# Kernel tuning notes

Measured on AMD Instinct MI355X. Metric: run time of the kernel, lower is better.

## Reference

```python
import jax, jax.numpy as jnp
import numpy as np

N = 100000       # nodes
E = 1600000      # edges (avg degree 16)
IN_DIM = 64
HID_DIM = 128
OUT_DIM = 64

def setup_inputs() -> dict:
    key = jax.random.key(0)
    k = jax.random.split(key, 8)
    inp = jax.random.normal(k[0], (IN_DIM, N), dtype=jnp.float32)
    src = jax.random.randint(k[1], (E,), 0, N, dtype=jnp.int32)
    dst = jax.random.randint(k[2], (E,), 0, N, dtype=jnp.int32)
    # Linear params (torch nn.Linear: y = x @ W.T + b)
    s1 = 1.0 / np.sqrt(IN_DIM)
    W1 = jax.random.uniform(k[3], (HID_DIM, IN_DIM), jnp.float32, -s1, s1)
    b1 = jax.random.uniform(k[4], (HID_DIM,), jnp.float32, -s1, s1)
    s2 = 1.0 / np.sqrt(HID_DIM)
    W2 = jax.random.uniform(k[5], (OUT_DIM, HID_DIM), jnp.float32, -s2, s2)
    b2 = jax.random.uniform(k[6], (OUT_DIM,), jnp.float32, -s2, s2)
    return {"inp": inp, "src": src, "dst": dst, "W1": W1, "b1": b1, "W2": W2, "b2": b2}

def reference(inp, src, dst, W1, b1, W2, b2):
    # inp: [in_dim, N] (module passes transposed features)
    X = inp.T                                   # [N, in_dim] node features
    # update_all(copy_src, sum): gather src features, scatter-add at dst
    agg = jax.ops.segment_sum(X[src], dst, num_segments=X.shape[0])  # [N, in_dim]
    h = jax.nn.relu(agg @ W1.T + b1)            # [N, hidden]
    out = h @ W2.T + b2                         # [N, out_dim]
    return out.T                                 # [out_dim, N] (final .t())
```

## Files before the change

### kernel.cpp

```cpp
#include <hip/hip_runtime.h>
#include <hip/hip_bf16.h>
#include <stdint.h>

typedef unsigned short ushort_t;
using short8   = __attribute__((ext_vector_type(8))) short;
using float4v  = __attribute__((ext_vector_type(4))) float;

#define BSH    6
#define BUCKW  64
#define CAP    1536
#define NBMAX  2048
#define TPITCH 266
#define BINB   128

__device__ __forceinline__ float bf2f(ushort_t u) {
    union { unsigned int i; float f; } v;
    v.i = ((unsigned int)u) << 16;
    return v.f;
}
__device__ __forceinline__ ushort_t f2b(float f) {
    union { float f; unsigned int i; } v;
    v.f = f;
    unsigned int u = v.i;
    unsigned int r = (u + 0x7fffu + ((u >> 16) & 1u)) >> 16;
    return (ushort_t)r;
}
__device__ __forceinline__ float blo2f(unsigned v) {
    union { unsigned i; float f; } u; u.i = v << 16; return u.f;
}
__device__ __forceinline__ float bhi2f(unsigned v) {
    union { unsigned i; float f; } u; u.i = v & 0xFFFF0000u; return u.f;
}

__global__ __launch_bounds__(1024) void prep_k(
        const float* __restrict__ inp, ushort_t* __restrict__ X, int N,
        const float* __restrict__ W1, const float* __restrict__ W2,
        ushort_t* __restrict__ w1b, ushort_t* __restrict__ w2b,
        const int* __restrict__ src, const int* __restrict__ dst,
        int* __restrict__ gcur, unsigned* __restrict__ bin, int E,
        int NB, int TB) {
    __shared__ __align__(16) char smem[64 * TPITCH * 2];
    int tid = threadIdx.x;

    if ((int)blockIdx.x < TB) {
        if (blockIdx.x == 0) {
            for (int i = tid; i < 8192; i += 1024) {
                w1b[i] = f2b(W1[i]);
                w2b[i] = f2b(W2[i]);
            }
        }
        ushort_t* tile = (ushort_t*)smem;
        int w    = tid >> 6;
        int lane = tid & 63;
        int n0   = blockIdx.x * 256;
        int col  = (w >> 2) * 64 + lane;
        int nc   = n0 + col;
#pragma unroll
        for (int r = 0; r < 16; ++r) {
            int d = (w & 3) * 16 + r;
            if (nc < N) tile[d * TPITCH + col] = f2b(inp[(size_t)d * N + nc]);
        }
        __syncthreads();
#pragma unroll
        for (int r = 0; r < 16; ++r) {
            int nl = w * 16 + r;
            int n  = n0 + nl;
            if (n < N) X[(size_t)n * 64 + lane] = tile[lane * TPITCH + nl];
        }
    } else {
        int* lcnt  = (int*)smem;
        int* gbase = lcnt + NBMAX;
        int* lcur  = gbase + NBMAX;
        int bid   = blockIdx.x - TB;
        int chunk = (E + BINB - 1) / BINB;
        int s0 = bid * chunk;
        int s1 = s0 + chunk;
        if (s1 > E) s1 = E;

        for (int b = tid; b < NB; b += 1024) lcnt[b] = 0;
        __syncthreads();

        for (int e = s0 + tid; e < s1; e += 1024)
            atomicAdd(&lcnt[dst[e] >> BSH], 1);
        __syncthreads();

        for (int b = tid; b < NB; b += 1024) {
            int c = lcnt[b];
            gbase[b] = c ? atomicAdd(&gcur[b], c) : 0;
            lcur[b]  = 0;
        }
        __syncthreads();

        for (int e = s0 + tid; e < s1; e += 1024) {
            int d = dst[e];
            int b = d >> BSH;
            int pos = gbase[b] + atomicAdd(&lcur[b], 1);
            if (pos < CAP)
                bin[(size_t)b * CAP + pos] =
                    ((unsigned)(d & (BUCKW - 1)) << 24) | (unsigned)src[e];
        }
    }
}

__global__ __launch_bounds__(256) void bagg_k(
        const unsigned* __restrict__ Xu, const unsigned* __restrict__ bin,
        const int* __restrict__ gcur, unsigned* __restrict__ aggu, int N) {
    __shared__ unsigned sl[CAP];
    __shared__ int ecnt[BUCKW];
    __shared__ int sc[BUCKW];
    __shared__ int ecur[BUCKW];
    int tid = threadIdx.x;
    int b   = blockIdx.x;
    int lo  = b << BSH;

    int cnt = gcur[b];
    if (cnt > CAP) cnt = CAP;
    const unsigned* bb = bin + (size_t)b * CAP;

    if (tid < BUCKW) ecnt[tid] = 0;
    __syncthreads();

    for (int i = tid; i < cnt; i += 256)
        atomicAdd(&ecnt[bb[i] >> 24], 1);
    __syncthreads();

    if (tid < BUCKW) sc[tid] = ecnt[tid];
    __syncthreads();
#pragma unroll
    for (int off = 1; off < BUCKW; off <<= 1) {
        int v = 0;
        if (tid < BUCKW && tid >= off) v = sc[tid - off];
        __syncthreads();
        if (tid < BUCKW) sc[tid] += v;
        __syncthreads();
    }
    if (tid < BUCKW) { sc[tid] -= ecnt[tid]; ecur[tid] = 0; }
    __syncthreads();

    for (int i = tid; i < cnt; i += 256) {
        unsigned p = bb[i];
        int nl  = (int)(p >> 24);
        int pos = sc[nl] + atomicAdd(&ecur[nl], 1);
        sl[pos] = p;
    }
    __syncthreads();

    int wave = tid >> 6;
    int lane = tid & 63;
    int half = lane >> 5;
    int c2   = lane & 31;

    for (int n = wave; n < BUCKW; n += 4) {
        int node = lo + n;
        if (node >= N) break;
        int s0 = sc[n];
        int c  = ecnt[n];
        float alo0 = 0.f, ahi0 = 0.f, alo1 = 0.f, ahi1 = 0.f;
        int i = 0;
        for (; i + 16 <= c; i += 16) {
            unsigned p0 = sl[s0 + i +  0 + half], p1 = sl[s0 + i +  2 + half];
            unsigned p2 = sl[s0 + i +  4 + half], p3 = sl[s0 + i +  6 + half];
            unsigned p4 = sl[s0 + i +  8 + half], p5 = sl[s0 + i + 10 + half];
            unsigned p6 = sl[s0 + i + 12 + half], p7 = sl[s0 + i + 14 + half];
            unsigned v0 = Xu[(size_t)(p0 & 0xFFFFFFu) * 32 + c2];
            unsigned v1 = Xu[(size_t)(p1 & 0xFFFFFFu) * 32 + c2];
            unsigned v2 = Xu[(size_t)(p2 & 0xFFFFFFu) * 32 + c2];
            unsigned v3 = Xu[(size_t)(p3 & 0xFFFFFFu) * 32 + c2];
            unsigned v4 = Xu[(size_t)(p4 & 0xFFFFFFu) * 32 + c2];
            unsigned v5 = Xu[(size_t)(p5 & 0xFFFFFFu) * 32 + c2];
            unsigned v6 = Xu[(size_t)(p6 & 0xFFFFFFu) * 32 + c2];
            unsigned v7 = Xu[(size_t)(p7 & 0xFFFFFFu) * 32 + c2];
            alo0 += blo2f(v0); ahi0 += bhi2f(v0);
            alo1 += blo2f(v1); ahi1 += bhi2f(v1);
            alo0 += blo2f(v2); ahi0 += bhi2f(v2);
            alo1 += blo2f(v3); ahi1 += bhi2f(v3);
            alo0 += blo2f(v4); ahi0 += bhi2f(v4);
            alo1 += blo2f(v5); ahi1 += bhi2f(v5);
            alo0 += blo2f(v6); ahi0 += bhi2f(v6);
            alo1 += blo2f(v7); ahi1 += bhi2f(v7);
        }
        for (; i + 2 <= c; i += 2) {
            unsigned p = sl[s0 + i + half];
            unsigned v = Xu[(size_t)(p & 0xFFFFFFu) * 32 + c2];
            alo0 += blo2f(v); ahi0 += bhi2f(v);
        }
        if (i + half < c) {
            unsigned p = sl[s0 + i + half];
            unsigned v = Xu[(size_t)(p & 0xFFFFFFu) * 32 + c2];
            alo1 += blo2f(v); ahi1 += bhi2f(v);
        }
        float alo = alo0 + alo1;
        float ahi = ahi0 + ahi1;
        float blo = __shfl(alo, lane + 32);
        float bhi = __shfl(ahi, lane + 32);
        if (half == 0) {
            alo += blo; ahi += bhi;
            aggu[(size_t)node * 32 + c2] =
                (unsigned)f2b(alo) | ((unsigned)f2b(ahi) << 16);
        }
    }
}

#define HPITCH 136

__global__ __launch_bounds__(256) void mlp_k(
        const ushort_t* __restrict__ aggb,
        const ushort_t* __restrict__ W1, const float* __restrict__ b1,
        const ushort_t* __restrict__ W2, const float* __restrict__ b2,
        float* __restrict__ out, int N) {
    __shared__ ushort_t h_s[4][16 * HPITCH];

    int wave = threadIdx.x >> 6;
    int lane = threadIdx.x & 63;
    int row  = lane & 15;
    int quad = lane >> 4;
    int n0   = blockIdx.x * 64 + wave * 16;

    int anode = n0 + row;
    if (anode > N - 1) anode = N - 1;
    const ushort_t* ap = aggb + (size_t)anode * 64;
    short8 a0 = *(const short8*)(ap + quad * 8);
    short8 a1 = *(const short8*)(ap + 32 + quad * 8);

    float4v zero = {0.f, 0.f, 0.f, 0.f};
    float4v acc[8];
#pragma unroll
    for (int nt = 0; nt < 8; ++nt) acc[nt] = zero;

#pragma unroll
    for (int nt = 0; nt < 8; ++nt) {
        const ushort_t* wp = W1 + (size_t)(nt * 16 + row) * 64 + quad * 8;
        short8 bf0 = *(const short8*)(wp);
        short8 bf1 = *(const short8*)(wp + 32);
        acc[nt] = __builtin_amdgcn_mfma_f32_16x16x32_bf16(a0, bf0, acc[nt], 0, 0, 0);
        acc[nt] = __builtin_amdgcn_mfma_f32_16x16x32_bf16(a1, bf1, acc[nt], 0, 0, 0);
    }

    ushort_t* hw = h_s[wave];
#pragma unroll
    for (int nt = 0; nt < 8; ++nt) {
        float bias = b1[nt * 16 + row];
#pragma unroll
        for (int r = 0; r < 4; ++r) {
            float v = acc[nt][r] + bias;
            v = v > 0.f ? v : 0.f;
            hw[(quad * 4 + r) * HPITCH + nt * 16 + row] = f2b(v);
        }
    }
    __syncthreads();

    short8 a2[4];
#pragma unroll
    for (int kt = 0; kt < 4; ++kt)
        a2[kt] = *(const short8*)(hw + row * HPITCH + kt * 32 + quad * 8);

    float4v acc2[4];
#pragma unroll
    for (int nt = 0; nt < 4; ++nt) acc2[nt] = zero;

#pragma unroll
    for (int nt = 0; nt < 4; ++nt) {
#pragma unroll
        for (int kt = 0; kt < 4; ++kt) {
            short8 bfr = *(const short8*)(W2 + (size_t)(nt * 16 + row) * 128 +
                                          kt * 32 + quad * 8);
            acc2[nt] = __builtin_amdgcn_mfma_f32_16x16x32_bf16(a2[kt], bfr, acc2[nt], 0, 0, 0);
        }
    }

    int node = n0 + quad * 4;
    if (node < N) {
#pragma unroll
        for (int nt = 0; nt < 4; ++nt) {
            int ko = nt * 16 + row;
            float bias = b2[ko];
            float4v pk;
#pragma unroll
            for (int r = 0; r < 4; ++r) pk[r] = acc2[nt][r] + bias;
            *(float4v*)(out + (size_t)ko * N + node) = pk;
        }
    }
}

extern "C" void kernel_launch(void* const* d_in, const int* in_sizes, int n_in,
                              void* d_out, int out_size, void* d_ws, size_t ws_size,
                              hipStream_t stream) {
    const float* inp = (const float*)d_in[0];
    const int*   src = (const int*)d_in[1];
    const int*   dst = (const int*)d_in[2];
    const float* W1  = (const float*)d_in[3];
    const float* b1  = (const float*)d_in[4];
    const float* W2  = (const float*)d_in[5];
    const float* b2  = (const float*)d_in[6];
    float* out = (float*)d_out;

    int N  = in_sizes[0] / 64;
    int E  = in_sizes[1];
    int NB = (N + BUCKW - 1) >> BSH;

    ushort_t* aggb = (ushort_t*)d_ws;
    ushort_t* w1b  = aggb + (size_t)N * 64;
    ushort_t* w2b  = w1b + 8192;
    int*      gcur = (int*)(w2b + 8192);

    char*     ob  = (char*)d_out;
    ushort_t* X   = (ushort_t*)ob;
    unsigned* bin = (unsigned*)(ob + (size_t)N * 64 * 2);

    hipMemsetAsync(gcur, 0, NB * sizeof(int), stream);

    int TB = (N + 255) / 256;
    prep_k<<<TB + BINB, 1024, 0, stream>>>(inp, X, N, W1, W2, w1b, w2b,
                                           src, dst, gcur, bin, E, NB, TB);

    bagg_k<<<NB, 256, 0, stream>>>((const unsigned*)X, bin, gcur,
                                   (unsigned*)aggb, N);

    int tb = (N + 63) / 64;
    mlp_k<<<tb, 256, 0, stream>>>(aggb, w1b, b1, w2b, b2, out, N);
}
```

Measured before the change: 204.1 us.

## Fuse aggregation with MLP via shared-memory tile and split prep kernels

Merges the bucket aggregation kernel with the MLP kernel, so each 64-node bucket's aggregated features go to LDS and feed the MFMA layers straight away instead of round-tripping through global memory. The transpose and binning work are split into separate kernels, and the memset is replaced by initialising gcur to absolute per-bucket offsets. This removes one global write and read of the aggregated features and one launch. In exchange, the binning no longer overlaps with the transpose, and the fused kernel's LDS use and register pressure grow.

```diff
diff --git a/kernel.cpp b/kernel.cpp
--- a/kernel.cpp
+++ b/kernel.cpp
@@ -10,8 +10,8 @@
 #define BUCKW  64
 #define CAP    1536
 #define NBMAX  2048
-#define TPITCH 266
-#define BINB   128
+#define HPITCH 136
+#define APITCH 72
 
 __device__ __forceinline__ float bf2f(ushort_t u) {
     union { unsigned int i; float f; } v;
@@ -32,92 +32,99 @@
     union { unsigned i; float f; } u; u.i = v & 0xFFFF0000u; return u.f;
 }
 
-__global__ __launch_bounds__(1024) void prep_k(
-        const float* __restrict__ inp, ushort_t* __restrict__ X, int N,
-        const float* __restrict__ W1, const float* __restrict__ W2,
-        ushort_t* __restrict__ w1b, ushort_t* __restrict__ w2b,
+__global__ void transpose_k(const float* __restrict__ inp,
+                            ushort_t* __restrict__ X, int N,
+                            const float* __restrict__ W1,
+                            const float* __restrict__ W2,
+                            ushort_t* __restrict__ w1b,
+                            ushort_t* __restrict__ w2b,
+                            int* __restrict__ gcur, int NB) {
+    if (blockIdx.x == 0) {
+        for (int i = threadIdx.x; i < 8192; i += 256) {
+            w1b[i] = f2b(W1[i]);
+            w2b[i] = f2b(W2[i]);
+        }
+        for (int b = threadIdx.x; b < NB; b += 256) gcur[b] = b * CAP;
+    }
+    __shared__ float tile[64][65];
+    int tx = threadIdx.x & 63;
+    int ty = threadIdx.x >> 6;
+    int n0 = blockIdx.x * 64;
+#pragma unroll
+    for (int r = 0; r < 16; ++r) {
+        int d = ty * 16 + r;
+        int n = n0 + tx;
+        if (n < N) tile[d][tx] = inp[(size_t)d * N + n];
+    }
+    __syncthreads();
+#pragma unroll
+    for (int r = 0; r < 16; ++r) {
+        int nl = ty * 16 + r;
+        int n  = n0 + nl;
+        if (n < N) X[(size_t)n * 64 + tx] = f2b(tile[tx][nl]);
+    }
+}
+
+__global__ __launch_bounds__(1024) void bin_k(
         const int* __restrict__ src, const int* __restrict__ dst,
-        int* __restrict__ gcur, unsigned* __restrict__ bin, int E,
-        int NB, int TB) {
-    __shared__ __align__(16) char smem[64 * TPITCH * 2];
-    int tid = threadIdx.x;
-
-    if ((int)blockIdx.x < TB) {
-        if (blockIdx.x == 0) {
-            for (int i = tid; i < 8192; i += 1024) {
-                w1b[i] = f2b(W1[i]);
-                w2b[i] = f2b(W2[i]);
-            }
-        }
-        ushort_t* tile = (ushort_t*)smem;
-        int w    = tid >> 6;
-        int lane = tid & 63;
-        int n0   = blockIdx.x * 256;
-        int col  = (w >> 2) * 64 + lane;
-        int nc   = n0 + col;
-#pragma unroll
-        for (int r = 0; r < 16; ++r) {
-            int d = (w & 3) * 16 + r;
-            if (nc < N) tile[d * TPITCH + col] = f2b(inp[(size_t)d * N + nc]);
-        }
-        __syncthreads();
-#pragma unroll
-        for (int r = 0; r < 16; ++r) {
-            int nl = w * 16 + r;
-            int n  = n0 + nl;
-            if (n < N) X[(size_t)n * 64 + lane] = tile[lane * TPITCH + nl];
-        }
-    } else {
-        int* lcnt  = (int*)smem;
-        int* gbase = lcnt + NBMAX;
-        int* lcur  = gbase + NBMAX;
-        int bid   = blockIdx.x - TB;
-        int chunk = (E + BINB - 1) / BINB;
-        int s0 = bid * chunk;
-        int s1 = s0 + chunk;
-        if (s1 > E) s1 = E;
-
-        for (int b = tid; b < NB; b += 1024) lcnt[b] = 0;
-        __syncthreads();
-
-        for (int e = s0 + tid; e < s1; e += 1024)
-            atomicAdd(&lcnt[dst[e] >> BSH], 1);
-        __syncthreads();
-
-        for (int b = tid; b < NB; b += 1024) {
-            int c = lcnt[b];
-            gbase[b] = c ? atomicAdd(&gcur[b], c) : 0;
-            lcur[b]  = 0;
-        }
-        __syncthreads();
-
-        for (int e = s0 + tid; e < s1; e += 1024) {
-            int d = dst[e];
-            int b = d >> BSH;
-            int pos = gbase[b] + atomicAdd(&lcur[b], 1);
-            if (pos < CAP)
-                bin[(size_t)b * CAP + pos] =
-                    ((unsigned)(d & (BUCKW - 1)) << 24) | (unsigned)src[e];
-        }
-    }
-}
-
-__global__ __launch_bounds__(256) void bagg_k(
+        int* __restrict__ gcur, unsigned* __restrict__ bin, int E, int NB) {
+    __shared__ int lcnt[NBMAX];
+    __shared__ int gbase[NBMAX];
+    __shared__ int lcur[NBMAX];
+    int tid   = threadIdx.x;
+    int chunk = (E + gridDim.x - 1) / gridDim.x;
+    int s0 = blockIdx.x * chunk;
+    int s1 = s0 + chunk;
+    if (s1 > E) s1 = E;
+
+    for (int b = tid; b < NB; b += 1024) lcnt[b] = 0;
+    __syncthreads();
+
+    for (int e = s0 + tid; e < s1; e += 1024)
+        atomicAdd(&lcnt[dst[e] >> BSH], 1);
+    __syncthreads();
+
+    for (int b = tid; b < NB; b += 1024) {
+        int c = lcnt[b];
+        gbase[b] = c ? atomicAdd(&gcur[b], c) : 0;
+        lcur[b]  = 0;
+    }
+    __syncthreads();
+
+    for (int e = s0 + tid; e < s1; e += 1024) {
+        int d = dst[e];
+        int b = d >> BSH;
+        int pos = gbase[b] + atomicAdd(&lcur[b], 1);
+        if (pos < (b + 1) * CAP)
+            bin[pos] = ((unsigned)(d & (BUCKW - 1)) << 24) | (unsigned)src[e];
+    }
+}
+
+__global__ __launch_bounds__(256) void baggmlp_k(
         const unsigned* __restrict__ Xu, const unsigned* __restrict__ bin,
-        const int* __restrict__ gcur, unsigned* __restrict__ aggu, int N) {
-    __shared__ unsigned sl[CAP];
-    __shared__ int ecnt[BUCKW];
-    __shared__ int sc[BUCKW];
-    __shared__ int ecur[BUCKW];
+        const int* __restrict__ gcur,
+        const ushort_t* __restrict__ W1, const float* __restrict__ b1,
+        const ushort_t* __restrict__ W2, const float* __restrict__ b2,
+        float* __restrict__ out, int N) {
+    __shared__ __align__(16) ushort_t agg_s[BUCKW * APITCH];
+    __shared__ __align__(16) char scratch[4 * 16 * HPITCH * 2];
+    unsigned* sl   = (unsigned*)scratch;
+    int*      ecnt = (int*)(scratch + CAP * 4);
+    int*      sc   = ecnt + BUCKW;
+    int*      ecur = sc + BUCKW;
+    ushort_t* h_s  = (ushort_t*)scratch;
+
     int tid = threadIdx.x;
     int b   = blockIdx.x;
     int lo  = b << BSH;
 
-    int cnt = gcur[b];
+    int cnt = gcur[b] - b * CAP;
     if (cnt > CAP) cnt = CAP;
     const unsigned* bb = bin + (size_t)b * CAP;
 
     if (tid < BUCKW) ecnt[tid] = 0;
+    for (int i = tid; i < BUCKW * (APITCH / 2); i += 256)
+        ((unsigned*)agg_s)[i] = 0;
     __syncthreads();
 
     for (int i = tid; i < cnt; i += 256)
@@ -191,34 +198,21 @@
         }
         float alo = alo0 + alo1;
         float ahi = ahi0 + ahi1;
-        float blo = __shfl(alo, lane + 32);
-        float bhi = __shfl(ahi, lane + 32);
+        float xlo = __shfl(alo, lane + 32);
+        float xhi = __shfl(ahi, lane + 32);
         if (half == 0) {
-            alo += blo; ahi += bhi;
-            aggu[(size_t)node * 32 + c2] =
+            alo += xlo; ahi += xhi;
+            ((unsigned*)agg_s)[n * (APITCH / 2) + c2] =
                 (unsigned)f2b(alo) | ((unsigned)f2b(ahi) << 16);
         }
     }
-}
-
-#define HPITCH 136
-
-__global__ __launch_bounds__(256) void mlp_k(
-        const ushort_t* __restrict__ aggb,
-        const ushort_t* __restrict__ W1, const float* __restrict__ b1,
-        const ushort_t* __restrict__ W2, const float* __restrict__ b2,
-        float* __restrict__ out, int N) {
-    __shared__ ushort_t h_s[4][16 * HPITCH];
-
-    int wave = threadIdx.x >> 6;
-    int lane = threadIdx.x & 63;
+    __syncthreads();
+
     int row  = lane & 15;
     int quad = lane >> 4;
-    int n0   = blockIdx.x * 64 + wave * 16;
-
-    int anode = n0 + row;
-    if (anode > N - 1) anode = N - 1;
-    const ushort_t* ap = aggb + (size_t)anode * 64;
+    int mloc = wave * 16 + row;
+
+    const ushort_t* ap = agg_s + mloc * APITCH;
     short8 a0 = *(const short8*)(ap + quad * 8);
     short8 a1 = *(const short8*)(ap + 32 + quad * 8);
 
@@ -236,7 +230,7 @@
         acc[nt] = __builtin_amdgcn_mfma_f32_16x16x32_bf16(a1, bf1, acc[nt], 0, 0, 0);
     }
 
-    ushort_t* hw = h_s[wave];
+    ushort_t* hw = h_s + wave * 16 * HPITCH;
 #pragma unroll
     for (int nt = 0; nt < 8; ++nt) {
         float bias = b1[nt * 16 + row];
@@ -268,7 +262,7 @@
         }
     }
 
-    int node = n0 + quad * 4;
+    int node = lo + wave * 16 + quad * 4;
     if (node < N) {
 #pragma unroll
         for (int nt = 0; nt < 4; ++nt) {
@@ -298,24 +292,16 @@
     int E  = in_sizes[1];
     int NB = (N + BUCKW - 1) >> BSH;
 
-    ushort_t* aggb = (ushort_t*)d_ws;
-    ushort_t* w1b  = aggb + (size_t)N * 64;
+    unsigned* bin  = (unsigned*)d_ws;
+    ushort_t* w1b  = (ushort_t*)((char*)d_ws + (size_t)NBMAX * CAP * 4);
     ushort_t* w2b  = w1b + 8192;
     int*      gcur = (int*)(w2b + 8192);
 
-    char*     ob  = (char*)d_out;
-    ushort_t* X   = (ushort_t*)ob;
-    unsigned* bin = (unsigned*)(ob + (size_t)N * 64 * 2);
-
-    hipMemsetAsync(gcur, 0, NB * sizeof(int), stream);
-
-    int TB = (N + 255) / 256;
-    prep_k<<<TB + BINB, 1024, 0, stream>>>(inp, X, N, W1, W2, w1b, w2b,
-                                           src, dst, gcur, bin, E, NB, TB);
-
-    bagg_k<<<NB, 256, 0, stream>>>((const unsigned*)X, bin, gcur,
-                                   (unsigned*)aggb, N);
+    ushort_t* X = (ushort_t*)(gcur + NBMAX);
 
     int tb = (N + 63) / 64;
-    mlp_k<<<tb, 256, 0, stream>>>(aggb, w1b, b1, w2b, b2, out, N);
-}
+    transpose_k<<<tb, 256, 0, stream>>>(inp, X, N, W1, W2, w1b, w2b, gcur, NB);
+    bin_k<<<128, 1024, 0, stream>>>(src, dst, gcur, bin, E, NB);
+    baggmlp_k<<<NB, 256, 0, stream>>>((const unsigned*)X, bin, gcur,
+                                      w1b, b1, w2b, b2, out, N);
+}
```

Result: slower. 212.6 us (+4.2%).
